# Optimization experiments

Measured on AMD Instinct MI355X. Metric: run time of the kernel, lower is better.

## Reference

```python
import jax, jax.numpy as jnp
import numpy as np

T, IN, M, C, OUT = 8192, 1024, 64, 16, 1024  # time, input, trace, context, output


def _ln(x, eps=1e-5):
    mu = jnp.mean(x, axis=-1, keepdims=True)
    var = jnp.var(x, axis=-1, keepdims=True)
    return (x - mu) * jax.lax.rsqrt(var + eps)


def _mish(x):
    return x * jnp.tanh(jax.nn.softplus(x))


def setup_inputs() -> dict:
    key = jax.random.key(0)
    ks = jax.random.split(key, 8)

    def w(k, o, i):
        return (jax.random.normal(k, (o, i), jnp.float32) / np.sqrt(i).astype(np.float32))

    return {
        "x": jax.random.normal(ks[0], (T, IN), jnp.float32),
        "state0": jnp.zeros((1, M, C), jnp.float32),  # real part of complex zero init
        "start": jax.random.uniform(ks[1], (T,)) < 0.002,  # sparse episode resets
        "next_done": jnp.zeros((T,), bool),  # unused by the sequential-equivalent math
        "a": jnp.linspace(1e-6, 0.5, M, dtype=jnp.float32),  # ffa.init decay
        "bf": (2.0 * jnp.pi / jnp.linspace(1.0, 1024.0, C)).astype(jnp.float32),  # ffa.init freqs
        "pre_w": w(ks[2], M, IN), "pre_b": jnp.zeros((M,), jnp.float32),
        "skip_w": w(ks[3], OUT, IN), "skip_b": jnp.zeros((OUT,), jnp.float32),
        "mix_w1": w(ks[4], M * C, 2 * M * C), "mix_b1": jnp.zeros((M * C,), jnp.float32),
        "mix_w2": w(ks[5], M * C, M * C), "mix_b2": jnp.zeros((M * C,), jnp.float32),
        "mix_w3": w(ks[6], OUT, M * C), "mix_b3": jnp.zeros((OUT,), jnp.float32),
    }


def _forward(x, state0, start, a, bf, pre_w, pre_b, skip_w, skip_b,
             mix_w1, mix_b1, mix_w2, mix_b2, mix_w3, mix_b3):
    Tn = x.shape[0]
    # pre = softplus(Linear(LayerNorm(x)))  -> [T, M]
    pre = jax.nn.softplus(_ln(x) @ pre_w.T + pre_b)
    # one-step FFA decay gamma[m,c] = exp(-|a_m| + i*b_c)
    la = jnp.broadcast_to(-jnp.abs(a)[:, None], (a.shape[0], bf.shape[0]))
    lb = jnp.broadcast_to(bf[None, :], la.shape)
    gamma = jnp.exp(jax.lax.complex(la, lb))  # [M, C] complex64
    # reset monoid: s_t = A_t * s_{t-1} + b_t,  A_t = 0 where episode starts
    A = jnp.where(start[:, None, None], jnp.zeros((), gamma.dtype), gamma[None])  # [T,M,C]
    b_el = jnp.broadcast_to(pre[:, :, None].astype(gamma.dtype), A.shape)  # [T,M,C]
    s_init = state0.astype(gamma.dtype)  # [1, M, C]
    b_el = b_el.at[0].add(A[0] * s_init[0])  # fold carried state into first element

    def combine(lhs, rhs):
        Al, bl = lhs
        Ar, br = rhs
        return Ar * Al, Ar * bl + br

    _, s = jax.lax.associative_scan(combine, (A, b_el))  # s: [T, M, C] states at every t

    s_flat = s.reshape(Tn, M * C)
    # global (all-element) complex mean / real std normalization, as in the source
    scaled = (s_flat - jnp.mean(s_flat)) / (1e-6 + jnp.std(s_flat))
    z = jnp.concatenate([scaled.real, scaled.imag], axis=-1)  # [T, 2*M*C]
    z = _mish(z @ mix_w1.T + mix_b1)
    z = _mish(z @ mix_w2.T + mix_b2)
    z = z @ mix_w3.T + mix_b3  # [T, OUT]
    out = _ln(z + (x @ skip_w.T + skip_b))
    return out, s[-1:]


def reference(x, state0, start, next_done, a, bf, pre_w, pre_b, skip_w, skip_b,
              mix_w1, mix_b1, mix_w2, mix_b2, mix_w3, mix_b3):
    return _forward(x, state0, start, a, bf, pre_w, pre_b, skip_w, skip_b,
                    mix_w1, mix_b1, mix_w2, mix_b2, mix_w3, mix_b3)
```

## Files before the change

kernel.cpp:

```cpp
#include <hip/hip_runtime.h>
#include <hip/hip_bf16.h>

#define T_    8192
#define INDIM 1024
#define MTR   64
#define CCTX  16
#define MC    1024
#define NOUT  1024
#define CHUNK 64
#define NCH   128

using bf16x8 = __attribute__((ext_vector_type(8))) short;
using f32x4  = __attribute__((ext_vector_type(4))) float;

__device__ __forceinline__ unsigned short f2bf(float f) {
  unsigned int u = __builtin_bit_cast(unsigned int, f);
  u += 0x7fffu + ((u >> 16) & 1u);
  return (unsigned short)(u >> 16);
}

__device__ __forceinline__ float mish_f(float v) {
  float u = __expf(v);
  float w = u * (u + 2.f);
  return (v > 20.f) ? v : v * __fdividef(w, w + 2.f);
}

typedef __attribute__((address_space(1))) void gas_void;
typedef __attribute__((address_space(3))) void las_void;

__device__ __forceinline__ void gload_lds16(const void* g, void* l) {
  __builtin_amdgcn_global_load_lds((gas_void*)g, (las_void*)l, 16, 0, 0);
}

__global__ __launch_bounds__(256) void cast4_k(const float* __restrict__ w1, const float* __restrict__ w2,
                                               const float* __restrict__ w3, const float* __restrict__ sw,
                                               unsigned short* __restrict__ o1, unsigned short* __restrict__ o2,
                                               unsigned short* __restrict__ o3, unsigned short* __restrict__ o4) {
  long i = ((long)blockIdx.x * 256 + threadIdx.x) * 4;
  const float* src; unsigned short* dst; long off;
  if (i < 2097152)      { src = w1; dst = o1; off = i; }
  else if (i < 3145728) { src = w2; dst = o2; off = i - 2097152; }
  else if (i < 4194304) { src = w3; dst = o3; off = i - 3145728; }
  else if (i < 5242880) { src = sw; dst = o4; off = i - 4194304; }
  else return;
  float4 v = *(const float4*)(src + off);
  ushort4 o = { f2bf(v.x), f2bf(v.y), f2bf(v.z), f2bf(v.w) };
  *(ushort4*)(dst + off) = o;
}

__device__ __forceinline__ float2 block_sum2(float s, float ss, float* sbuf) {
#pragma unroll
  for (int off = 32; off > 0; off >>= 1) {
    s  += __shfl_down(s, off);
    ss += __shfl_down(ss, off);
  }
  if ((threadIdx.x & 63) == 0) {
    sbuf[(threadIdx.x >> 6) * 2]     = s;
    sbuf[(threadIdx.x >> 6) * 2 + 1] = ss;
  }
  __syncthreads();
  return make_float2(sbuf[0] + sbuf[2] + sbuf[4] + sbuf[6],
                     sbuf[1] + sbuf[3] + sbuf[5] + sbuf[7]);
}

__global__ __launch_bounds__(256) void ln_cast_k(const float* __restrict__ x,
                                                 float2* __restrict__ rowstat,
                                                 unsigned short* __restrict__ xb) {
  __shared__ float sbuf[8];
  const long row = blockIdx.x;
  float4 v = ((const float4*)(x + (row << 10)))[threadIdx.x];
  ushort4 c = { f2bf(v.x), f2bf(v.y), f2bf(v.z), f2bf(v.w) };
  ((ushort4*)(xb + (row << 10)))[threadIdx.x] = c;
  float2 t = block_sum2(v.x + v.y + v.z + v.w,
                        v.x * v.x + v.y * v.y + v.z * v.z + v.w * v.w, sbuf);
  float mean = t.x * (1.f / 1024.f);
  float var  = t.y * (1.f / 1024.f) - mean * mean;
  float rstd = rsqrtf(var + 1e-5f);
  if (threadIdx.x == 0) rowstat[row] = make_float2(mean, rstd);
}

__global__ __launch_bounds__(256) void ln_out1_k(const float* __restrict__ p, float* __restrict__ out) {
  __shared__ float sbuf[8];
  const long row = blockIdx.x;
  float4 v = ((const float4*)(p + (row << 10)))[threadIdx.x];
  float2 t = block_sum2(v.x + v.y + v.z + v.w,
                        v.x * v.x + v.y * v.y + v.z * v.z + v.w * v.w, sbuf);
  float mean = t.x * (1.f / 1024.f);
  float var  = t.y * (1.f / 1024.f) - mean * mean;
  float rstd = rsqrtf(var + 1e-5f);
  float4 o = { (v.x - mean) * rstd, (v.y - mean) * rstd,
               (v.z - mean) * rstd, (v.w - mean) * rstd };
  ((float4*)(out + (row << 10)))[threadIdx.x] = o;
}

__global__ __launch_bounds__(256) void pre_part_k(const float* __restrict__ x,
                                                  const float2* __restrict__ rowstat,
                                                  const float* __restrict__ pw,
                                                  float* __restrict__ part) {
  const int lane = threadIdx.x & 63;
  const int wvu  = __builtin_amdgcn_readfirstlane(threadIdx.x >> 6);
  const int kc   = blockIdx.y;
  const int r0   = (blockIdx.x * 4 + wvu) * 32;

  const float* wrow = pw + (long)lane * 1024 + kc * 128;
  float wreg[128];
#pragma unroll
  for (int j = 0; j < 32; ++j)
    *(float4*)&wreg[j * 4] = ((const float4*)wrow)[j];
  float swsum = 0.f;
#pragma unroll
  for (int j = 0; j < 128; ++j) swsum += wreg[j];

  float* po = part + ((long)kc * T_ + r0) * 64 + lane;
  const float* xbase = x + (long)r0 * 1024 + kc * 128;

  for (int i = 0; i < 32; i += 2) {
    const float4* xr0 = (const float4*)(xbase + (long)i * 1024);
    const float4* xr1 = (const float4*)(xbase + (long)(i + 1) * 1024);
    float a0 = 0.f, a1 = 0.f, a2 = 0.f, a3 = 0.f;
    float b0 = 0.f, b1 = 0.f, b2 = 0.f, b3 = 0.f;
#pragma unroll
    for (int j = 0; j < 32; j += 4) {
      float4 xa0 = xr0[j],     xa1 = xr0[j + 1], xa2 = xr0[j + 2], xa3 = xr0[j + 3];
      float4 xb0 = xr1[j],     xb1 = xr1[j + 1], xb2 = xr1[j + 2], xb3 = xr1[j + 3];
      a0 += wreg[4*j+0]*xa0.x  + wreg[4*j+1]*xa0.y  + wreg[4*j+2]*xa0.z  + wreg[4*j+3]*xa0.w;
      a1 += wreg[4*j+4]*xa1.x  + wreg[4*j+5]*xa1.y  + wreg[4*j+6]*xa1.z  + wreg[4*j+7]*xa1.w;
      a2 += wreg[4*j+8]*xa2.x  + wreg[4*j+9]*xa2.y  + wreg[4*j+10]*xa2.z + wreg[4*j+11]*xa2.w;
      a3 += wreg[4*j+12]*xa3.x + wreg[4*j+13]*xa3.y + wreg[4*j+14]*xa3.z + wreg[4*j+15]*xa3.w;
      b0 += wreg[4*j+0]*xb0.x  + wreg[4*j+1]*xb0.y  + wreg[4*j+2]*xb0.z  + wreg[4*j+3]*xb0.w;
      b1 += wreg[4*j+4]*xb1.x  + wreg[4*j+5]*xb1.y  + wreg[4*j+6]*xb1.z  + wreg[4*j+7]*xb1.w;
      b2 += wreg[4*j+8]*xb2.x  + wreg[4*j+9]*xb2.y  + wreg[4*j+10]*xb2.z + wreg[4*j+11]*xb2.w;
      b3 += wreg[4*j+12]*xb3.x + wreg[4*j+13]*xb3.y + wreg[4*j+14]*xb3.z + wreg[4*j+15]*xb3.w;
    }
    float2 s0 = rowstat[r0 + i];
    float2 s1 = rowstat[r0 + i + 1];
    po[(long)i * 64]       = s0.y * ((a0 + a1) + (a2 + a3)) - s0.x * s0.y * swsum;
    po[(long)(i + 1) * 64] = s1.y * ((b0 + b1) + (b2 + b3)) - s1.x * s1.y * swsum;
  }
}

__global__ __launch_bounds__(256) void pre_fin_k(const float* __restrict__ part,
                                                 const float* __restrict__ pb,
                                                 float* __restrict__ pre) {
  long i = (long)blockIdx.x * 256 + threadIdx.x;
  int m = (int)(i & 63);
  float s = 0.f;
#pragma unroll
  for (int kc = 0; kc < 8; ++kc)
    s += part[(long)kc * T_ * 64 + i];
  float v = s + pb[m];
  float sp = fmaxf(v, 0.f) + log1pf(expf(-fabsf(v)));
  pre[i] = sp;
}

__global__ __launch_bounds__(256) void scan_p1(const float* __restrict__ pre, const int* __restrict__ start,
                                               const float* __restrict__ a, const float* __restrict__ bfr,
                                               double2* __restrict__ chA, double2* __restrict__ chB) {
  int ch = blockIdx.y * 256 + threadIdx.x;
  int m = ch >> 4, c = ch & 15;
  double dec = exp(-fabs((double)a[m]));
  double th = (double)bfr[c];
  double gre = dec * cos(th), gim = dec * sin(th);
  int j = blockIdx.x;
  int t0 = j * CHUNK;
  double pr = 1.0, pi = 0.0, sr = 0.0, si = 0.0;
  for (int t = t0; t < t0 + CHUNK; ++t) {
    double b = (double)pre[(long)t * 64 + m];
    if (start[t]) {
      pr = 0.0; pi = 0.0; sr = b; si = 0.0;
    } else {
      double nsr = gre * sr - gim * si + b;
      si = gre * si + gim * sr; sr = nsr;
      double npr = gre * pr - gim * pi;
      pi = gre * pi + gim * pr; pr = npr;
    }
  }
  chA[j * MC + ch] = make_double2(pr, pi);
  chB[j * MC + ch] = make_double2(sr, si);
}

__global__ __launch_bounds__(64) void scan_p2(const double2* __restrict__ chA, const double2* __restrict__ chB,
                                              const float* __restrict__ state0,
                                              double2* __restrict__ carry, double* __restrict__ red,
                                              float* __restrict__ out_tail, int fmt) {
  if (blockIdx.x == 0 && threadIdx.x < 4) red[threadIdx.x] = 0.0;
  int ch = blockIdx.x * 64 + threadIdx.x;
  double cr = (double)state0[ch], ci = 0.0;
  for (int j = 0; j < NCH; ++j) {
    carry[j * MC + ch] = make_double2(cr, ci);
    double2 A = chA[j * MC + ch];
    double2 B = chB[j * MC + ch];
    double ncr = A.x * cr - A.y * ci + B.x;
    ci = A.x * ci + A.y * cr + B.y;
    cr = ncr;
  }
  if (fmt == 1024) {
    out_tail[ch] = (float)cr;
  } else {
    out_tail[2 * ch]     = (float)cr;
    out_tail[2 * ch + 1] = (float)ci;
  }
}

__global__ __launch_bounds__(256) void scan_p3(const float* __restrict__ pre, const int* __restrict__ start,
                                               const float* __restrict__ a, const float* __restrict__ bfr,
                                               const double2* __restrict__ carry,
                                               double* __restrict__ red) {
  __shared__ double sbuf[12];
  int ch = blockIdx.y * 256 + threadIdx.x;
  int m = ch >> 4, c = ch & 15;
  double dec = exp(-fabs((double)a[m]));
  double th = (double)bfr[c];
  double gre = dec * cos(th), gim = dec * sin(th);
  int j = blockIdx.x;
  int t0 = j * CHUNK;
  double2 cin = carry[j * MC + ch];
  double sr = cin.x, si = cin.y;
  double aR = 0.0, aI = 0.0, aS = 0.0;
  for (int t = t0; t < t0 + CHUNK; ++t) {
    double b = (double)pre[(long)t * 64 + m];
    if (start[t]) { sr = b; si = 0.0; }
    else {
      double nsr = gre * sr - gim * si + b;
      si = gre * si + gim * sr; sr = nsr;
    }
    aR += sr; aI += si; aS += sr * sr + si * si;
  }
#pragma unroll
  for (int off = 32; off > 0; off >>= 1) {
    aR += __shfl_down(aR, off); aI += __shfl_down(aI, off); aS += __shfl_down(aS, off);
  }
  if ((threadIdx.x & 63) == 0) {
    int w = threadIdx.x >> 6;
    sbuf[w * 3] = aR; sbuf[w * 3 + 1] = aI; sbuf[w * 3 + 2] = aS;
  }
  __syncthreads();
  if (threadIdx.x == 0) {
    atomicAdd(&red[0], sbuf[0] + sbuf[3] + sbuf[6] + sbuf[9]);
    atomicAdd(&red[1], sbuf[1] + sbuf[4] + sbuf[7] + sbuf[10]);
    atomicAdd(&red[2], sbuf[2] + sbuf[5] + sbuf[8] + sbuf[11]);
  }
}

__global__ void finalize_red(const double* __restrict__ red, float* __restrict__ redf) {
  const double n = (double)T_ * (double)MC;
  double mre = red[0] / n, mim = red[1] / n;
  double var = red[2] / n - mre * mre - mim * mim;
  double sd = sqrt(var > 0.0 ? var : 0.0);
  redf[0] = (float)mre;
  redf[1] = (float)mim;
  redf[2] = (float)(1.0 / (1e-6 + sd));
}

__global__ __launch_bounds__(256) void zscan_k(const float* __restrict__ pre, const int* __restrict__ start,
                                               const float* __restrict__ a, const float* __restrict__ bfr,
                                               const double2* __restrict__ carry, const float* __restrict__ redf,
                                               unsigned short* __restrict__ z) {
  int ch = blockIdx.y * 256 + threadIdx.x;
  int m = ch >> 4, c = ch & 15;
  double dec = exp(-fabs((double)a[m]));
  double th = (double)bfr[c];
  double gre = dec * cos(th), gim = dec * sin(th);
  int j = blockIdx.x;
  int t0 = j * CHUNK;
  double2 cin = carry[j * MC + ch];
  double sr = cin.x, si = cin.y;
  const float mre = redf[0], mim = redf[1], inv = redf[2];
  for (int t = t0; t < t0 + CHUNK; ++t) {
    double b = (double)pre[(long)t * 64 + m];
    if (start[t]) { sr = b; si = 0.0; }
    else {
      double nsr = gre * sr - gim * si + b;
      si = gre * si + gim * sr; sr = nsr;
    }
    z[(long)t * 2048 + ch]        = f2bf(((float)sr - mre) * inv);
    z[(long)t * 2048 + 1024 + ch] = f2bf(((float)si - mim) * inv);
  }
}

#define TSZ (128 * 32)
template<int EP>
__device__ __forceinline__ void gemm128_core(const unsigned short* __restrict__ A,
                                             const unsigned short* __restrict__ B,
                                             const float* __restrict__ bias,
                                             const float* __restrict__ add,
                                             void* __restrict__ Cout,
                                             int bx, int by, int N_, int K_,
                                             unsigned short* lA, unsigned short* lB) {
  const int tid = threadIdx.x;
  const int lane = tid & 63;
  const int wv = tid >> 6;
  const int wr = wv >> 1, wc = wv & 1;
  const long brow = (long)bx * 128;
  const long bcol = (long)by * 128;

  f32x4 acc[4][4];
#pragma unroll
  for (int i = 0; i < 4; i++)
#pragma unroll
    for (int j = 0; j < 4; j++)
      acc[i][j] = f32x4{0.f, 0.f, 0.f, 0.f};

  const int c0 = tid, c1 = tid + 256;
  const long ar0 = brow + (c0 >> 2), ar1 = brow + (c1 >> 2);
  const long br0 = bcol + (c0 >> 2), br1 = bcol + (c1 >> 2);
  const int ko0 = (((c0 & 3) ^ ((c0 >> 3) & 3)) * 8);
  const int ko1 = (((c1 & 3) ^ ((c1 >> 3) & 3)) * 8);
  const int r15 = lane & 15;
  const int swzq = (((lane >> 4) ^ ((r15 >> 1) & 3)) * 8);

  const int nt = K_ >> 5;

#define STAGE(ti, bu)                                                      \
  do {                                                                     \
    gload_lds16(A + ar0 * K_ + (ti) * 32 + ko0, lA + (bu) * TSZ + c0 * 8); \
    gload_lds16(A + ar1 * K_ + (ti) * 32 + ko1, lA + (bu) * TSZ + c1 * 8); \
    gload_lds16(B + br0 * K_ + (ti) * 32 + ko0, lB + (bu) * TSZ + c0 * 8); \
    gload_lds16(B + br1 * K_ + (ti) * 32 + ko1, lB + (bu) * TSZ + c1 * 8); \
  } while (0)

  STAGE(0, 0);
  STAGE(1, 1);
  STAGE(2, 2);

  for (int i = 0; i < nt; ++i) {
    if (i + 3 < nt) {
      STAGE(i + 3, (i + 3) & 3);
      asm volatile("s_waitcnt vmcnt(12)" ::: "memory");
    } else {
      int r = nt - 1 - i;
      if (r == 2)      asm volatile("s_waitcnt vmcnt(8)" ::: "memory");
      else if (r == 1) asm volatile("s_waitcnt vmcnt(4)" ::: "memory");
      else             asm volatile("s_waitcnt vmcnt(0)" ::: "memory");
    }
    __builtin_amdgcn_sched_barrier(0);
    __builtin_amdgcn_s_barrier();
    __builtin_amdgcn_sched_barrier(0);

    const unsigned short* bA = lA + (i & 3) * TSZ;
    const unsigned short* bB = lB + (i & 3) * TSZ;
    bf16x8 af[4], bv[4];
#pragma unroll
    for (int mi = 0; mi < 4; mi++)
      af[mi] = *(const bf16x8*)&bA[(wr * 64 + mi * 16 + r15) * 32 + swzq];
#pragma unroll
    for (int nj = 0; nj < 4; nj++)
      bv[nj] = *(const bf16x8*)&bB[(wc * 64 + nj * 16 + r15) * 32 + swzq];
#pragma unroll
    for (int mi = 0; mi < 4; mi++)
#pragma unroll
      for (int nj = 0; nj < 4; nj++)
        acc[mi][nj] = __builtin_amdgcn_mfma_f32_16x16x32_bf16(af[mi], bv[nj], acc[mi][nj], 0, 0, 0);

    __builtin_amdgcn_sched_barrier(0);
    __builtin_amdgcn_s_barrier();
  }
#undef STAGE

  const int rq = (lane >> 4) * 4;
#pragma unroll
  for (int nj = 0; nj < 4; nj++) {
    const long col = bcol + wc * 64 + nj * 16 + r15;
    const float bs = bias[col];
#pragma unroll
    for (int mi = 0; mi < 4; mi++) {
#pragma unroll
      for (int r = 0; r < 4; r++) {
        const long row = brow + wr * 64 + mi * 16 + rq + r;
        float v = acc[mi][nj][r] + bs;
        if (EP == 0) {
          ((float*)Cout)[row * N_ + col] = v;
        } else if (EP == 3) {
          ((float*)Cout)[row * N_ + col] = v + add[row * N_ + col];
        } else {
          ((unsigned short*)Cout)[row * N_ + col] = f2bf(mish_f(v));
        }
      }
    }
  }
}

template<int EP>
__global__ __launch_bounds__(256) void gemm128_k(const unsigned short* __restrict__ A,
                                                 const unsigned short* __restrict__ B,
                                                 const float* __restrict__ bias,
                                                 const float* __restrict__ add,
                                                 void* __restrict__ Cout, int N_, int K_) {
  __shared__ __align__(16) unsigned short lA[4 * TSZ];
  __shared__ __align__(16) unsigned short lB[4 * TSZ];
  gemm128_core<EP>(A, B, bias, add, Cout, blockIdx.x, blockIdx.y, N_, K_, lA, lB);
}

__global__ __launch_bounds__(256) void gemm_dual128(const unsigned short* __restrict__ A1,
                                                    const unsigned short* __restrict__ B1,
                                                    const float* __restrict__ bias1,
                                                    unsigned short* __restrict__ C1, int K1,
                                                    const unsigned short* __restrict__ A2,
                                                    const unsigned short* __restrict__ B2,
                                                    const float* __restrict__ bias2,
                                                    float* __restrict__ C2, int K2) {
  __shared__ __align__(16) unsigned short lA[4 * TSZ];
  __shared__ __align__(16) unsigned short lB[4 * TSZ];
  int b = blockIdx.x;
  if (b < 512) {
    gemm128_core<2>(A1, B1, bias1, nullptr, C1, b & 63, b >> 6, 1024, K1, lA, lB);
  } else {
    b -= 512;
    gemm128_core<0>(A2, B2, bias2, nullptr, C2, b & 63, b >> 6, 1024, K2, lA, lB);
  }
}

extern "C" void kernel_launch(void* const* d_in, const int* in_sizes, int n_in,
                              void* d_out, int out_size, void* d_ws, size_t ws_size,
                              hipStream_t stream) {
  (void)in_sizes; (void)n_in; (void)ws_size;
  const float* x      = (const float*)d_in[0];
  const float* state0 = (const float*)d_in[1];
  const int*   start  = (const int*)d_in[2];
  const float* a      = (const float*)d_in[4];
  const float* bfr    = (const float*)d_in[5];
  const float* pre_w  = (const float*)d_in[6];
  const float* pre_b  = (const float*)d_in[7];
  const float* skip_w = (const float*)d_in[8];
  const float* skip_b = (const float*)d_in[9];
  const float* w1     = (const float*)d_in[10];
  const float* b1     = (const float*)d_in[11];
  const float* w2     = (const float*)d_in[12];
  const float* b2     = (const float*)d_in[13];
  const float* w3     = (const float*)d_in[14];
  const float* b3     = (const float*)d_in[15];

  char* ws = (char*)d_ws;
  const size_t MB = 1u << 20;
  float*          skipf = (float*)(ws + 0);
  float*          part  = (float*)(ws + 32 * MB);
  float*          h3    = (float*)(ws + 32 * MB);
  unsigned short* z     = (unsigned short*)(ws + 64 * MB);
  unsigned short* xb    = (unsigned short*)(ws + 96 * MB);
  unsigned short* h2    = (unsigned short*)(ws + 96 * MB);
  unsigned short* h1    = (unsigned short*)(ws + 112 * MB);
  unsigned short* wb1   = (unsigned short*)(ws + 128 * MB);
  unsigned short* wb2   = (unsigned short*)(ws + 132 * MB);
  unsigned short* wb3   = (unsigned short*)(ws + 134 * MB);
  unsigned short* skwb  = (unsigned short*)(ws + 136 * MB);
  float*          pre   = (float*)(ws + 138 * MB);
  double2*        chA   = (double2*)(ws + 140 * MB);
  double2*        chB   = (double2*)(ws + 142 * MB);
  double2*        carry = (double2*)(ws + 144 * MB);
  double*         red   = (double*)(ws + 146 * MB);
  float*          redf  = (float*)(ws + 146 * MB + 64);
  float2*         rowst = (float2*)(ws + 147 * MB);

  cast4_k<<<5120, 256, 0, stream>>>(w1, w2, w3, skip_w, wb1, wb2, wb3, skwb);

  ln_cast_k<<<8192, 256, 0, stream>>>(x, rowst, xb);
  pre_part_k<<<dim3(64, 8), 256, 0, stream>>>(x, rowst, pre_w, part);
  pre_fin_k<<<2048, 256, 0, stream>>>(part, pre_b, pre);

  int tail_elems = out_size - T_ * NOUT;
  float* out_tail = (float*)d_out + (long)T_ * NOUT;
  scan_p1<<<dim3(NCH, 4), 256, 0, stream>>>(pre, start, a, bfr, chA, chB);
  scan_p2<<<16, 64, 0, stream>>>(chA, chB, state0, carry, red, out_tail, tail_elems);
  scan_p3<<<dim3(NCH, 4), 256, 0, stream>>>(pre, start, a, bfr, carry, red);
  finalize_red<<<1, 1, 0, stream>>>(red, redf);

  zscan_k<<<dim3(NCH, 4), 256, 0, stream>>>(pre, start, a, bfr, carry, redf, z);

  gemm_dual128<<<1024, 256, 0, stream>>>(z, wb1, b1, h1, 2048, xb, skwb, skip_b, skipf, 1024);
  gemm128_k<2><<<dim3(64, 8), 256, 0, stream>>>(h1, wb2, b2, nullptr, h2, 1024, 1024);
  gemm128_k<3><<<dim3(64, 8), 256, 0, stream>>>(h2, wb3, b3, skipf, h3, 1024, 1024);

  ln_out1_k<<<8192, 256, 0, stream>>>(h3, (float*)d_out);
}
```

Baseline: 302.5 us.

## Fold global scan normalization into first GEMM epilogue and drop second scan pass

Writes unnormalized bf16 scan states directly in the reduction pass and removes the separate rescan kernel that applied mean/std normalization. The normalization is applied algebraically in the first MLP GEMM's epilogue using precomputed per-output row sums of the real and imaginary halves of w1. GEMM LDS buffering is also reduced from four to three stages with a two-deep prefetch. This risks bf16 precision loss because the uncentered states are quantized before the mean is subtracted.

```diff
diff --git a/kernel.cpp b/kernel.cpp
--- a/kernel.cpp
+++ b/kernel.cpp
@@ -61,6 +61,17 @@
   __syncthreads();
   return make_float2(sbuf[0] + sbuf[2] + sbuf[4] + sbuf[6],
                      sbuf[1] + sbuf[3] + sbuf[5] + sbuf[7]);
+}
+
+__global__ __launch_bounds__(256) void wsum_k(const float* __restrict__ w1,
+                                              float* __restrict__ wre, float* __restrict__ wim) {
+  __shared__ float sbuf[8];
+  const long row = blockIdx.x;
+  const float4* r4 = (const float4*)(w1 + row * 2048);
+  float4 a = r4[threadIdx.x];
+  float4 b = r4[256 + threadIdx.x];
+  float2 t = block_sum2(a.x + a.y + a.z + a.w, b.x + b.y + b.z + b.w, sbuf);
+  if (threadIdx.x == 0) { wre[row] = t.x; wim[row] = t.y; }
 }
 
 __global__ __launch_bounds__(256) void ln_cast_k(const float* __restrict__ x,
@@ -205,7 +216,8 @@
 __global__ __launch_bounds__(256) void scan_p3(const float* __restrict__ pre, const int* __restrict__ start,
                                                const float* __restrict__ a, const float* __restrict__ bfr,
                                                const double2* __restrict__ carry,
-                                               double* __restrict__ red) {
+                                               double* __restrict__ red,
+                                               unsigned short* __restrict__ z) {
   __shared__ double sbuf[12];
   int ch = blockIdx.y * 256 + threadIdx.x;
   int m = ch >> 4, c = ch & 15;
@@ -224,6 +236,8 @@
       double nsr = gre * sr - gim * si + b;
       si = gre * si + gim * sr; sr = nsr;
     }
+    z[(long)t * 2048 + ch]        = f2bf((float)sr);
+    z[(long)t * 2048 + 1024 + ch] = f2bf((float)si);
     aR += sr; aI += si; aS += sr * sr + si * si;
   }
 #pragma unroll
@@ -252,38 +266,15 @@
   redf[2] = (float)(1.0 / (1e-6 + sd));
 }
 
-__global__ __launch_bounds__(256) void zscan_k(const float* __restrict__ pre, const int* __restrict__ start,
-                                               const float* __restrict__ a, const float* __restrict__ bfr,
-                                               const double2* __restrict__ carry, const float* __restrict__ redf,
-                                               unsigned short* __restrict__ z) {
-  int ch = blockIdx.y * 256 + threadIdx.x;
-  int m = ch >> 4, c = ch & 15;
-  double dec = exp(-fabs((double)a[m]));
-  double th = (double)bfr[c];
-  double gre = dec * cos(th), gim = dec * sin(th);
-  int j = blockIdx.x;
-  int t0 = j * CHUNK;
-  double2 cin = carry[j * MC + ch];
-  double sr = cin.x, si = cin.y;
-  const float mre = redf[0], mim = redf[1], inv = redf[2];
-  for (int t = t0; t < t0 + CHUNK; ++t) {
-    double b = (double)pre[(long)t * 64 + m];
-    if (start[t]) { sr = b; si = 0.0; }
-    else {
-      double nsr = gre * sr - gim * si + b;
-      si = gre * si + gim * sr; sr = nsr;
-    }
-    z[(long)t * 2048 + ch]        = f2bf(((float)sr - mre) * inv);
-    z[(long)t * 2048 + 1024 + ch] = f2bf(((float)si - mim) * inv);
-  }
-}
-
 #define TSZ (128 * 32)
 template<int EP>
 __device__ __forceinline__ void gemm128_core(const unsigned short* __restrict__ A,
                                              const unsigned short* __restrict__ B,
                                              const float* __restrict__ bias,
                                              const float* __restrict__ add,
+                                             const float* __restrict__ redf,
+                                             const float* __restrict__ wre,
+                                             const float* __restrict__ wim,
                                              void* __restrict__ Cout,
                                              int bx, int by, int N_, int K_,
                                              unsigned short* lA, unsigned short* lB) {
@@ -321,24 +312,23 @@
 
   STAGE(0, 0);
   STAGE(1, 1);
-  STAGE(2, 2);
-
+
+  int use = 0, stg = 2;
   for (int i = 0; i < nt; ++i) {
-    if (i + 3 < nt) {
-      STAGE(i + 3, (i + 3) & 3);
-      asm volatile("s_waitcnt vmcnt(12)" ::: "memory");
+    if (i + 2 < nt) {
+      STAGE(i + 2, stg);
+      asm volatile("s_waitcnt vmcnt(8)" ::: "memory");
+    } else if (i + 1 < nt) {
+      asm volatile("s_waitcnt vmcnt(4)" ::: "memory");
     } else {
-      int r = nt - 1 - i;
-      if (r == 2)      asm volatile("s_waitcnt vmcnt(8)" ::: "memory");
-      else if (r == 1) asm volatile("s_waitcnt vmcnt(4)" ::: "memory");
-      else             asm volatile("s_waitcnt vmcnt(0)" ::: "memory");
+      asm volatile("s_waitcnt vmcnt(0)" ::: "memory");
     }
     __builtin_amdgcn_sched_barrier(0);
     __builtin_amdgcn_s_barrier();
     __builtin_amdgcn_sched_barrier(0);
 
-    const unsigned short* bA = lA + (i & 3) * TSZ;
-    const unsigned short* bB = lB + (i & 3) * TSZ;
+    const unsigned short* bA = lA + use * TSZ;
+    const unsigned short* bB = lB + use * TSZ;
     bf16x8 af[4], bv[4];
 #pragma unroll
     for (int mi = 0; mi < 4; mi++)
@@ -354,26 +344,36 @@
 
     __builtin_amdgcn_sched_barrier(0);
     __builtin_amdgcn_s_barrier();
+    use = (use == 2) ? 0 : use + 1;
+    stg = (stg == 2) ? 0 : stg + 1;
   }
 #undef STAGE
+
+  float cre = 0.f, cim = 0.f, inv = 1.f;
+  if (EP == 4) { cre = redf[0]; cim = redf[1]; inv = redf[2]; }
 
   const int rq = (lane >> 4) * 4;
 #pragma unroll
   for (int nj = 0; nj < 4; nj++) {
     const long col = bcol + wc * 64 + nj * 16 + r15;
     const float bs = bias[col];
+    float wrc = 0.f, wic = 0.f;
+    if (EP == 4) { wrc = wre[col]; wic = wim[col]; }
 #pragma unroll
     for (int mi = 0; mi < 4; mi++) {
 #pragma unroll
       for (int r = 0; r < 4; r++) {
         const long row = brow + wr * 64 + mi * 16 + rq + r;
-        float v = acc[mi][nj][r] + bs;
+        float va = acc[mi][nj][r];
         if (EP == 0) {
-          ((float*)Cout)[row * N_ + col] = v;
+          ((float*)Cout)[row * N_ + col] = va + bs;
         } else if (EP == 3) {
-          ((float*)Cout)[row * N_ + col] = v + add[row * N_ + col];
+          ((float*)Cout)[row * N_ + col] = va + bs + add[row * N_ + col];
+        } else if (EP == 4) {
+          float v = (va - cre * wrc - cim * wic) * inv + bs;
+          ((unsigned short*)Cout)[row * N_ + col] = f2bf(mish_f(v));
         } else {
-          ((unsigned short*)Cout)[row * N_ + col] = f2bf(mish_f(v));
+          ((unsigned short*)Cout)[row * N_ + col] = f2bf(mish_f(va + bs));
         }
       }
     }
@@ -386,27 +386,31 @@
                                                  const float* __restrict__ bias,
                                                  const float* __restrict__ add,
                                                  void* __restrict__ Cout, int N_, int K_) {
-  __shared__ __align__(16) unsigned short lA[4 * TSZ];
-  __shared__ __align__(16) unsigned short lB[4 * TSZ];
-  gemm128_core<EP>(A, B, bias, add, Cout, blockIdx.x, blockIdx.y, N_, K_, lA, lB);
+  __shared__ __align__(16) unsigned short lA[3 * TSZ];
+  __shared__ __align__(16) unsigned short lB[3 * TSZ];
+  gemm128_core<EP>(A, B, bias, add, nullptr, nullptr, nullptr, Cout,
+                   blockIdx.x, blockIdx.y, N_, K_, lA, lB);
 }
 
 __global__ __launch_bounds__(256) void gemm_dual128(const unsigned short* __restrict__ A1,
                                                     const unsigned short* __restrict__ B1,
                                                     const float* __restrict__ bias1,
                                                     unsigned short* __restrict__ C1, int K1,
+                                                    const float* __restrict__ redf,
+                                                    const float* __restrict__ wre,
+                                                    const float* __restrict__ wim,
                                                     const unsigned short* __restrict__ A2,
                                                     const unsigned short* __restrict__ B2,
                                                     const float* __restrict__ bias2,
                                                     float* __restrict__ C2, int K2) {
-  __shared__ __align__(16) unsigned short lA[4 * TSZ];
-  __shared__ __align__(16) unsigned short lB[4 * TSZ];
+  __shared__ __align__(16) unsigned short lA[3 * TSZ];
+  __shared__ __align__(16) unsigned short lB[3 * TSZ];
   int b = blockIdx.x;
   if (b < 512) {
-    gemm128_core<2>(A1, B1, bias1, nullptr, C1, b & 63, b >> 6, 1024, K1, lA, lB);
+    gemm128_core<4>(A1, B1, bias1, nullptr, redf, wre, wim, C1, b & 63, b >> 6, 1024, K1, lA, lB);
   } else {
     b -= 512;
-    gemm128_core<0>(A2, B2, bias2, nullptr, C2, b & 63, b >> 6, 1024, K2, lA, lB);
+    gemm128_core<0>(A2, B2, bias2, nullptr, nullptr, nullptr, nullptr, C2, b & 63, b >> 6, 1024, K2, lA, lB);
   }
 }
 
@@ -450,8 +454,11 @@
   double*         red   = (double*)(ws + 146 * MB);
   float*          redf  = (float*)(ws + 146 * MB + 64);
   float2*         rowst = (float2*)(ws + 147 * MB);
+  float*          wre   = (float*)(ws + 147 * MB + 65536);
+  float*          wim   = (float*)(ws + 147 * MB + 65536 + 4096);
 
   cast4_k<<<5120, 256, 0, stream>>>(w1, w2, w3, skip_w, wb1, wb2, wb3, skwb);
+  wsum_k<<<1024, 256, 0, stream>>>(w1, wre, wim);
 
   ln_cast_k<<<8192, 256, 0, stream>>>(x, rowst, xb);
   pre_part_k<<<dim3(64, 8), 256, 0, stream>>>(x, rowst, pre_w, part);
@@ -461,12 +468,11 @@
   float* out_tail = (float*)d_out + (long)T_ * NOUT;
   scan_p1<<<dim3(NCH, 4), 256, 0, stream>>>(pre, start, a, bfr, chA, chB);
   scan_p2<<<16, 64, 0, stream>>>(chA, chB, state0, carry, red, out_tail, tail_elems);
-  scan_p3<<<dim3(NCH, 4), 256, 0, stream>>>(pre, start, a, bfr, carry, red);
+  scan_p3<<<dim3(NCH, 4), 256, 0, stream>>>(pre, start, a, bfr, carry, red, z);
   finalize_red<<<1, 1, 0, stream>>>(red, redf);
 
-  zscan_k<<<dim3(NCH, 4), 256, 0, stream>>>(pre, start, a, bfr, carry, redf, z);
-
-  gemm_dual128<<<1024, 256, 0, stream>>>(z, wb1, b1, h1, 2048, xb, skwb, skip_b, skipf, 1024);
+  gemm_dual128<<<1024, 256, 0, stream>>>(z, wb1, b1, h1, 2048, redf, wre, wim,
+                                         xb, skwb, skip_b, skipf, 1024);
   gemm128_k<2><<<dim3(64, 8), 256, 0, stream>>>(h1, wb2, b2, nullptr, h2, 1024, 1024);
   gemm128_k<3><<<dim3(64, 8), 256, 0, stream>>>(h2, wb3, b3, skipf, h3, 1024, 1024);
 
```

After: 296.7 us. No clear change (-1.9%).
